# Optimization experiments

Hardware: AMD Instinct MI355X
Metric: run time of the kernel (lower is better)

## Reference

```python
import jax, jax.numpy as jnp
import numpy as np

B, L = 8, 1024
VOCAB = 5000
DW = 256            # d_word_vec = d_model
H = 3 * DW          # hidden_size = 768
NH, HD = 12, 64     # n_head, d_k
D = NH * HD         # 768 = nhead*head_dim
D_INNER = 3072
N_LAYERS = 2
N_HIDDEN = 1024
N_OUT = 5000
MASK = 0
SCALE = 1.0 / float(np.sqrt(HD))


def _sinusoid(n_pos, d_hid):
    pos = np.arange(n_pos, dtype=np.float64)[:, None]
    hid = np.arange(d_hid)[None, :]
    tab = pos / np.power(10000.0, 2 * (hid // 2) / d_hid)
    tab[:, 0::2] = np.sin(tab[:, 0::2])
    tab[:, 1::2] = np.cos(tab[:, 1::2])
    tab[0] = 0.0  # padding_idx=0
    return jnp.asarray(tab, dtype=jnp.float32)


def _ln(x, g, b, eps=1e-5):
    mu = x.mean(-1, keepdims=True)
    var = ((x - mu) ** 2).mean(-1, keepdims=True)
    return (x - mu) * jax.lax.rsqrt(var + eps) * g + b


def _dense(x, w, b):
    # w: [out, in] (torch Conv 1x1 / Linear convention)
    return jnp.einsum('...i,oi->...o', x, w) + b


def _pwff(x, w1, b1, w2, b2, g, bn):
    out = _dense(jax.nn.relu(_dense(x, w1, b1)), w2, b2)
    return _ln(out + x, g, bn)


def _msa1(x, relay, wq, bq, wk, bk, wv, bv, wo, bo):
    # x: [B, L, H] nodes, relay: [B, H]. Star-Transformer ring attention:
    # window = 3 local neighbors + the relay node (4 keys per query).
    Bx, Lx, _ = x.shape
    q = _dense(x, wq, bq).reshape(Bx, Lx, NH, HD)
    k = _dense(x, wk, bk).reshape(Bx, Lx, NH, HD)
    v = _dense(x, wv, bv).reshape(Bx, Lx, NH, HD)
    kp = jnp.pad(k, ((0, 0), (1, 1), (0, 0), (0, 0)))
    vp = jnp.pad(v, ((0, 0), (1, 1), (0, 0), (0, 0)))
    k_win = jnp.stack([kp[:, u:u + Lx] for u in range(3)], axis=2)  # [B,L,3,NH,HD]
    v_win = jnp.stack([vp[:, u:u + Lx] for u in range(3)], axis=2)
    rk = _dense(relay, wk, bk).reshape(Bx, NH, HD)
    rv = _dense(relay, wv, bv).reshape(Bx, NH, HD)
    s_loc = jnp.einsum('blnh,blwnh->blwn', q, k_win)
    s_rel = jnp.einsum('blnh,bnh->bln', q, rk)
    scores = jnp.concatenate([s_loc, s_rel[:, :, None, :]], axis=2) * SCALE  # [B,L,4,NH]
    a = jax.nn.softmax(scores, axis=2)
    att = jnp.einsum('blwn,blwnh->blnh', a[:, :, :3], v_win) + a[:, :, 3][..., None] * rv[:, None]
    return _dense(att.reshape(Bx, Lx, D), wo, bo)


def _msa2(relay, nodes, smask, wq, bq, wk, bk, wv, bv, wo, bo):
    # Satellite->planet global attention: single query (relay) over [relay; nodes].
    Bx = relay.shape[0]
    y = jnp.concatenate([relay[:, None, :], nodes], axis=1)  # [B, 1+L, H]
    q = _dense(relay, wq, bq).reshape(Bx, NH, HD)
    k = _dense(y, wk, bk).reshape(Bx, -1, NH, HD)
    v = _dense(y, wv, bv).reshape(Bx, -1, NH, HD)
    pre = jnp.einsum('bnh,bsnh->bns', q, k) * SCALE
    pre = jnp.where(smask[:, None, :], -jnp.inf, pre)
    a = jax.nn.softmax(pre, axis=2)
    att = jnp.einsum('bns,bsnh->bnh', a, v).reshape(Bx, D)
    return _dense(att, wo, bo)


def setup_inputs():
    ks = iter(jax.random.split(jax.random.key(0), 40))
    def w(shape):
        return jax.random.normal(next(ks), shape, dtype=jnp.float32) * 0.02
    def z(shape):
        return jnp.zeros(shape, jnp.float32)
    def o(shape):
        return jnp.ones(shape, jnp.float32)
    inp = {}
    inp['src_seq'] = jax.random.randint(next(ks), (B, L, 3), 0, VOCAB, dtype=jnp.int32)
    inp['positions'] = jax.random.randint(next(ks), (B,), 0, L, dtype=jnp.int32)
    inp['emb'] = w((VOCAB, DW))
    inp['pos_table'] = _sinusoid(L, H)
    inp['norm_g'] = o((N_LAYERS, H)); inp['norm_b'] = z((N_LAYERS, H))
    inp['pw_w1'] = w((N_LAYERS, D_INNER, H)); inp['pw_b1'] = z((N_LAYERS, D_INNER))
    inp['pw_w2'] = w((N_LAYERS, H, D_INNER)); inp['pw_b2'] = z((N_LAYERS, H))
    inp['pw_g'] = o((N_LAYERS, H)); inp['pw_bn'] = z((N_LAYERS, H))
    for p in ['ring', 'star']:
        inp[p + '_wq'] = w((N_LAYERS, D, H)); inp[p + '_bq'] = z((N_LAYERS, D))
        inp[p + '_wk'] = w((N_LAYERS, D, H)); inp[p + '_bk'] = z((N_LAYERS, D))
        inp[p + '_wv'] = w((N_LAYERS, D, H)); inp[p + '_bv'] = z((N_LAYERS, D))
        inp[p + '_wo'] = w((N_LAYERS, H, D)); inp[p + '_bo'] = z((N_LAYERS, H))
    inp['head_w1'] = w((3, N_HIDDEN, 2 * H)); inp['head_b1'] = z((3, N_HIDDEN))
    inp['head_w2'] = w((3, N_OUT, N_HIDDEN)); inp['head_b2'] = z((3, N_OUT))
    return inp


def reference(src_seq, positions, emb, pos_table, norm_g, norm_b, pw_w1, pw_b1, pw_w2, pw_b2, pw_g, pw_bn, ring_wq, ring_bq, ring_wk, ring_bk, ring_wv, ring_bv, ring_wo, ring_bo, star_wq, star_bq, star_wk, star_bk, star_wv, star_bv, star_wo, star_bo, head_w1, head_b1, head_w2, head_b2):
    Bx, Lx, _ = src_seq.shape
    # [B,L,3,DW] -> [B,L,H], add (frozen) sinusoid positional encoding
    x = emb[src_seq].reshape(Bx, Lx, H) + pos_table[None, :Lx]
    mask_pad = src_seq[:, :, 0] == MASK               # True at padded positions
    smask = jnp.concatenate([jnp.zeros((Bx, 1), bool), mask_pad], axis=1)
    nodes = x
    relay = x.mean(axis=1)                            # [B, H]
    for i in range(N_LAYERS):
        h = _pwff(nodes, pw_w1[i], pw_b1[i], pw_w2[i], pw_b2[i], pw_g[i], pw_bn[i])
        ring = _msa1(h, relay, ring_wq[i], ring_bq[i], ring_wk[i], ring_bk[i], ring_wv[i], ring_bv[i], ring_wo[i], ring_bo[i])
        nodes = jax.nn.leaky_relu(_ln(ring, norm_g[i], norm_b[i]))
        relay = jax.nn.leaky_relu(_msa2(relay, nodes, smask, star_wq[i], star_bq[i], star_wk[i], star_bk[i], star_wv[i], star_bv[i], star_wo[i], star_bo[i]))
        nodes = jnp.where(mask_pad[:, :, None], 0.0, nodes)
    target = nodes[jnp.arange(Bx), positions]         # [B, H]
    ft = jnp.concatenate([relay, target], axis=1)     # [B, 2H]
    outs = [_dense(jax.nn.relu(_dense(ft, head_w1[j], head_b1[j])), head_w2[j], head_b2[j]) for j in range(3)]
    return jnp.concatenate(outs, axis=1).reshape(3 * Bx, N_OUT)
```

## Files before the change

kernel.cpp:

```cpp
#include <hip/hip_runtime.h>
#include <cstdint>
#include <cstddef>


typedef unsigned short u16;
typedef __attribute__((ext_vector_type(4))) float f32x4;
typedef __attribute__((ext_vector_type(8))) __bf16 bf16x8;

#define NB 8
#define SEQ 1024
#define HDIM 768
#define NHEAD 12
#define HD 64
#define DINNER 3072
#define NHID 1024
#define NOUT 5000
#define ATT_SCALE 0.125f

static __device__ __forceinline__ float b2f(u16 u) {
  union { float f; uint32_t i; } v; v.i = ((uint32_t)u) << 16; return v.f;
}
static __device__ __forceinline__ u16 f2b(float f) {
  union { float f; uint32_t i; } v; v.f = f;
  uint32_t r = v.i + 0x7fffu + ((v.i >> 16) & 1u);
  return (u16)(r >> 16);
}
static __device__ __forceinline__ float2 b2f2(uint32_t u) {
  union { float f; uint32_t i; } lo, hi;
  lo.i = u << 16; hi.i = u & 0xffff0000u;
  return make_float2(lo.f, hi.f);
}

static __device__ __forceinline__ void gl2lds16(const void* g, void* l) {
  __builtin_amdgcn_global_load_lds(
      (__attribute__((address_space(1))) void*)(uintptr_t)g,
      (__attribute__((address_space(3))) void*)l, 16, 0, 0);
}

template <int N>
static __device__ __forceinline__ void wait_vmcnt() {
  if constexpr (N == 0) asm volatile("s_waitcnt vmcnt(0)" ::: "memory");
  else if constexpr (N == 3) asm volatile("s_waitcnt vmcnt(3)" ::: "memory");
  else if constexpr (N == 4) asm volatile("s_waitcnt vmcnt(4)" ::: "memory");
  else if constexpr (N == 6) asm volatile("s_waitcnt vmcnt(6)" ::: "memory");
  else if constexpr (N == 8) asm volatile("s_waitcnt vmcnt(8)" ::: "memory");
}

static __device__ __forceinline__ float blk_sum(float v, float* red) {
  #pragma unroll
  for (int off = 32; off > 0; off >>= 1) v += __shfl_down(v, off, 64);
  if ((threadIdx.x & 63) == 0) red[threadIdx.x >> 6] = v;
  __syncthreads();
  float r = red[0] + red[1] + red[2] + red[3];
  __syncthreads();
  return r;
}
static __device__ __forceinline__ float blk_max(float v, float* red) {
  #pragma unroll
  for (int off = 32; off > 0; off >>= 1) v = fmaxf(v, __shfl_down(v, off, 64));
  if ((threadIdx.x & 63) == 0) red[threadIdx.x >> 6] = v;
  __syncthreads();
  float r = fmaxf(fmaxf(red[0], red[1]), fmaxf(red[2], red[3]));
  __syncthreads();
  return r;
}

struct Cvt4 {
  const float* s0; const float* s1; const float* s2; const float* s3;
  u16* d0; u16* d1; u16* d2; u16* d3;
  int c1, c2, c3, c4;
};
__global__ __launch_bounds__(256) void cvt4_k(Cvt4 a) {
  const int i = blockIdx.x * 256 + threadIdx.x;
  if (i >= a.c4) return;
  const float* s; u16* d; int j;
  if (i < a.c1)      { s = a.s0; d = a.d0; j = i; }
  else if (i < a.c2) { s = a.s1; d = a.d1; j = i - a.c1; }
  else if (i < a.c3) { s = a.s2; d = a.d2; j = i - a.c2; }
  else               { s = a.s3; d = a.d3; j = i - a.c3; }
  const float4 v = ((const float4*)s)[j];
  ushort4 o;
  o.x = f2b(v.x); o.y = f2b(v.y); o.z = f2b(v.z); o.w = f2b(v.w);
  ((ushort4*)d)[j] = o;
}

template <int ACT, int TM>
__global__ __launch_bounds__(256) void gemm_bt(
    const u16* __restrict__ A,
    const u16* W0, const u16* W1, const u16* W2,
    const float* b0, const float* b1, const float* b2,
    u16* C0, u16* C1, u16* C2,
    int M, int N, int K) {
  constexpr int MI = TM / 32;
  constexpr int S = TM / 64 + 2;
  __shared__ u16 As[4][TM * 32];
  __shared__ u16 Bs[4][128 * 32];
  const int z = blockIdx.z;
  const u16* W = z == 0 ? W0 : (z == 1 ? W1 : W2);
  const float* bias = z == 0 ? b0 : (z == 1 ? b1 : b2);
  u16* C = z == 0 ? C0 : (z == 1 ? C1 : C2);

  const int tid  = threadIdx.x;
  const int wave = tid >> 6;
  const int lane = tid & 63;
  const int bm = blockIdx.y * TM;
  const int bn = blockIdx.x * 128;
  const int wrq = wave >> 1, wcq = wave & 1;
  const int r16 = lane & 15, quad = lane >> 4;
  const int srow = lane >> 2;
  const int scol = (lane & 3) << 3;

  f32x4 acc[MI][4] = {};

  const int nk = K >> 5;

  auto STAGE = [&](int s, int t) {
    const int k0 = t << 5;
    #pragma unroll
    for (int q = 0; q < TM / 64; ++q) {
      const int rowa = wave * (TM / 4) + q * 16;
      gl2lds16(A + (size_t)(bm + rowa + srow) * K + (k0 + scol),
               (char*)&As[s][0] + (rowa << 6));
    }
    #pragma unroll
    for (int q = 0; q < 2; ++q) {
      const int rowb = wave * 32 + q * 16;
      gl2lds16(W + (size_t)(bn + rowb + srow) * K + (k0 + scol),
               (char*)&Bs[s][0] + (rowb << 6));
    }
  };

  STAGE(0, 0);
  if (1 < nk) STAGE(1, 1);

  for (int t = 0; t < nk; ++t) {
    const int s = t & 3;
    if (t + 2 < nk) {
      STAGE((t + 2) & 3, t + 2);
      __builtin_amdgcn_sched_barrier(0);
      wait_vmcnt<2 * S>();
    } else if (t + 1 < nk) {
      wait_vmcnt<S>();
    } else {
      wait_vmcnt<0>();
    }
    __builtin_amdgcn_sched_barrier(0);
    __builtin_amdgcn_s_barrier();
    __builtin_amdgcn_sched_barrier(0);

    bf16x8 af[MI], bf[4];
    #pragma unroll
    for (int i = 0; i < MI; ++i)
      af[i] = *reinterpret_cast<const bf16x8*>(
          &As[s][(wrq * (TM / 2) + i * 16 + r16) * 32 + quad * 8]);
    #pragma unroll
    for (int j = 0; j < 4; ++j)
      bf[j] = *reinterpret_cast<const bf16x8*>(
          &Bs[s][(wcq * 64 + j * 16 + r16) * 32 + quad * 8]);
    #pragma unroll
    for (int i = 0; i < MI; ++i)
      #pragma unroll
      for (int j = 0; j < 4; ++j)
        acc[i][j] = __builtin_amdgcn_mfma_f32_16x16x32_bf16(af[i], bf[j], acc[i][j], 0, 0, 0);
  }

  #pragma unroll
  for (int j = 0; j < 4; ++j) {
    const int n = bn + wcq * 64 + j * 16 + r16;
    const float bv = bias[n];
    #pragma unroll
    for (int i = 0; i < MI; ++i) {
      const int m0 = bm + wrq * (TM / 2) + i * 16 + quad * 4;
      #pragma unroll
      for (int r = 0; r < 4; ++r) {
        float vv = acc[i][j][r] + bv;
        if (ACT == 1) vv = fmaxf(vv, 0.0f);
        C[(size_t)(m0 + r) * N + n] = f2b(vv);
      }
    }
  }
}

__global__ __launch_bounds__(256) void embed_k(
    const int* __restrict__ src, const float* __restrict__ emb,
    const float* __restrict__ pt, float* __restrict__ x,
    u16* __restrict__ xb) {
  const int r = blockIdx.x;
  const int l = r & (SEQ - 1);
  const int tid = threadIdx.x;
  #pragma unroll
  for (int it = 0; it < 3; ++it) {
    const int idx = tid + it * 256;
    const int c = idx >> 8, d = idx & 255;
    const int tok = src[r * 3 + c];
    const float v = emb[(size_t)tok * 256 + d] + pt[(size_t)l * HDIM + idx];
    x[(size_t)r * HDIM + idx] = v;
    xb[(size_t)r * HDIM + idx] = f2b(v);
  }
}

__global__ __launch_bounds__(256) void relay_mean1_k(
    const float* __restrict__ x, float* __restrict__ part) {
  const int cg = blockIdx.x, seg = blockIdx.y, b = blockIdx.z;
  const int h = cg * 256 + threadIdx.x;
  float s = 0.f;
  const int l0 = seg * 64;
  for (int l = l0; l < l0 + 64; ++l) s += x[((size_t)b * SEQ + l) * HDIM + h];
  part[((size_t)b * 16 + seg) * HDIM + h] = s;
}
__global__ __launch_bounds__(256) void relay_mean2_k(
    const float* __restrict__ part, float* __restrict__ relay) {
  const int b = blockIdx.y;
  const int h = blockIdx.x * 256 + threadIdx.x;
  float s = 0.f;
  #pragma unroll
  for (int i = 0; i < 16; ++i) s += part[((size_t)b * 16 + i) * HDIM + h];
  relay[b * HDIM + h] = s * (1.0f / 1024.0f);
}

__global__ __launch_bounds__(256) void ln_resid_k(
    const u16* __restrict__ pre, const float* __restrict__ res,
    const float* __restrict__ g, const float* __restrict__ bb,
    u16* __restrict__ out) {
  __shared__ float red[4];
  const int r = blockIdx.x;
  const int tid = threadIdx.x;
  const size_t base = (size_t)r * HDIM;
  float v0 = b2f(pre[base + tid])       + res[base + tid];
  float v1 = b2f(pre[base + tid + 256]) + res[base + tid + 256];
  float v2 = b2f(pre[base + tid + 512]) + res[base + tid + 512];
  const float mu = blk_sum(v0 + v1 + v2, red) * (1.0f / 768.0f);
  v0 -= mu; v1 -= mu; v2 -= mu;
  const float var = blk_sum(v0 * v0 + v1 * v1 + v2 * v2, red) * (1.0f / 768.0f);
  const float rs = rsqrtf(var + 1e-5f);
  out[base + tid]       = f2b(v0 * rs * g[tid]       + bb[tid]);
  out[base + tid + 256] = f2b(v1 * rs * g[tid + 256] + bb[tid + 256]);
  out[base + tid + 512] = f2b(v2 * rs * g[tid + 512] + bb[tid + 512]);
}

__global__ __launch_bounds__(256) void ln_leaky_mask_k(
    const u16* __restrict__ pre, const float* __restrict__ g,
    const float* __restrict__ bb, const int* __restrict__ src,
    float* __restrict__ out, u16* __restrict__ outb) {
  __shared__ float red[4];
  const int r = blockIdx.x;
  const int tid = threadIdx.x;
  const size_t base = (size_t)r * HDIM;
  float v0 = b2f(pre[base + tid]);
  float v1 = b2f(pre[base + tid + 256]);
  float v2 = b2f(pre[base + tid + 512]);
  const float mu = blk_sum(v0 + v1 + v2, red) * (1.0f / 768.0f);
  v0 -= mu; v1 -= mu; v2 -= mu;
  const float var = blk_sum(v0 * v0 + v1 * v1 + v2 * v2, red) * (1.0f / 768.0f);
  const float rs = rsqrtf(var + 1e-5f);
  const bool masked = (src[r * 3] == 0);
  float y0 = v0 * rs * g[tid]       + bb[tid];
  float y1 = v1 * rs * g[tid + 256] + bb[tid + 256];
  float y2 = v2 * rs * g[tid + 512] + bb[tid + 512];
  y0 = y0 > 0.f ? y0 : 0.01f * y0;
  y1 = y1 > 0.f ? y1 : 0.01f * y1;
  y2 = y2 > 0.f ? y2 : 0.01f * y2;
  if (masked) { y0 = 0.f; y1 = 0.f; y2 = 0.f; }
  out[base + tid]       = y0;  outb[base + tid]       = f2b(y0);
  out[base + tid + 256] = y1;  outb[base + tid + 256] = f2b(y1);
  out[base + tid + 512] = y2;  outb[base + tid + 512] = f2b(y2);
}

__global__ __launch_bounds__(256) void ring_attn_k(
    const u16* __restrict__ q, const u16* __restrict__ k,
    const u16* __restrict__ v, const float* __restrict__ rk,
    const float* __restrict__ rv, u16* __restrict__ att) {
  __shared__ float qs[HDIM];
  __shared__ float aw[NHEAD][4];
  const int r = blockIdx.x;
  const int b = r >> 10, l = r & (SEQ - 1);
  const int tid = threadIdx.x;
  const size_t base = (size_t)r * HDIM;
  #pragma unroll
  for (int it = 0; it < 3; ++it) {
    const int idx = tid + it * 256;
    qs[idx] = b2f(q[base + idx]);
  }
  __syncthreads();
  if (tid < 192) {
    const int u_ = tid >> 2;
    const int l4 = tid & 3;
    const int n = u_ >> 2, w = u_ & 3;
    const float* qrow = qs + n * HD + l4 * 16;
    float a = 0.f;
    if (w < 3) {
      const int ll = l - 1 + w;
      if (ll >= 0 && ll < SEQ) {
        const uint4* kp4 =
            (const uint4*)(k + base + (size_t)(w - 1) * HDIM + n * HD + l4 * 16);
        #pragma unroll
        for (int t = 0; t < 2; ++t) {
          const uint4 u = kp4[t];
          const float2 f0 = b2f2(u.x), f1 = b2f2(u.y);
          const float2 f2_ = b2f2(u.z), f3 = b2f2(u.w);
          const float* q8 = qrow + t * 8;
          a += q8[0] * f0.x + q8[1] * f0.y + q8[2] * f1.x + q8[3] * f1.y
             + q8[4] * f2_.x + q8[5] * f2_.y + q8[6] * f3.x + q8[7] * f3.y;
        }
      }
    } else {
      const float4* kp4 = (const float4*)(rk + b * HDIM + n * HD + l4 * 16);
      #pragma unroll
      for (int t = 0; t < 4; ++t) {
        const float4 kv = kp4[t];
        const float* q4 = qrow + t * 4;
        a += q4[0] * kv.x + q4[1] * kv.y + q4[2] * kv.z + q4[3] * kv.w;
      }
    }
    a += __shfl_xor(a, 1, 4);
    a += __shfl_xor(a, 2, 4);
    if (l4 == 0) aw[n][w] = a * ATT_SCALE;
  }
  __syncthreads();
  if (tid < NHEAD) {
    const float s0 = aw[tid][0], s1 = aw[tid][1], s2 = aw[tid][2], s3 = aw[tid][3];
    const float m = fmaxf(fmaxf(s0, s1), fmaxf(s2, s3));
    const float e0 = __expf(s0 - m), e1 = __expf(s1 - m);
    const float e2 = __expf(s2 - m), e3 = __expf(s3 - m);
    const float inv = 1.0f / (e0 + e1 + e2 + e3);
    aw[tid][0] = e0 * inv; aw[tid][1] = e1 * inv;
    aw[tid][2] = e2 * inv; aw[tid][3] = e3 * inv;
  }
  __syncthreads();
  #pragma unroll
  for (int it = 0; it < 3; ++it) {
    const int idx = tid + it * 256;
    const int n = idx >> 6;
    float acc = aw[n][3] * rv[b * HDIM + idx];
    if (l > 0)       acc += aw[n][0] * b2f(v[base - HDIM + idx]);
    acc += aw[n][1] * b2f(v[base + idx]);
    if (l < SEQ - 1) acc += aw[n][2] * b2f(v[base + HDIM + idx]);
    att[base + idx] = f2b(acc);
  }
}

__global__ __launch_bounds__(256) void msa2_attn_k(
    const float* __restrict__ q2, const float* __restrict__ rk2,
    const float* __restrict__ rv2, const u16* __restrict__ k2,
    const u16* __restrict__ v2, const int* __restrict__ src,
    float* __restrict__ att) {
  __shared__ float qs[HD];
  __shared__ float sc[SEQ + 1];
  __shared__ float red[4];
  __shared__ float vred[4][HD];
  const int bid = blockIdx.x;
  const int b = bid / NHEAD, n = bid % NHEAD;
  const int tid = threadIdx.x;
  const int hb = b * HDIM + n * HD;
  if (tid < HD) qs[tid] = q2[hb + tid];
  __syncthreads();
  float lmax = -1e30f;
  for (int s = tid; s <= SEQ; s += 256) {
    float sco;
    if (s == 0) {
      float a = 0.f;
      #pragma unroll
      for (int d = 0; d < HD; ++d) a += qs[d] * rk2[hb + d];
      sco = a * ATT_SCALE;
    } else {
      const int l = s - 1;
      if (src[(b * SEQ + l) * 3] == 0) {
        sco = -1e30f;
      } else {
        const uint4* kp4 =
            (const uint4*)(k2 + ((size_t)b * SEQ + l) * HDIM + n * HD);
        float a = 0.f;
        #pragma unroll
        for (int t = 0; t < 8; ++t) {
          const uint4 u = kp4[t];
          const float2 f0 = b2f2(u.x), f1 = b2f2(u.y);
          const float2 f2_ = b2f2(u.z), f3 = b2f2(u.w);
          const float* q8 = qs + t * 8;
          a += q8[0] * f0.x + q8[1] * f0.y + q8[2] * f1.x + q8[3] * f1.y
             + q8[4] * f2_.x + q8[5] * f2_.y + q8[6] * f3.x + q8[7] * f3.y;
        }
        sco = a * ATT_SCALE;
      }
    }
    sc[s] = sco;
    lmax = fmaxf(lmax, sco);
  }
  lmax = blk_max(lmax, red);
  float lsum = 0.f;
  for (int s = tid; s <= SEQ; s += 256) {
    const float e = __expf(sc[s] - lmax);
    sc[s] = e;
    lsum += e;
  }
  lsum = blk_sum(lsum, red);
  {
    const int dd = tid & 63, grp = tid >> 6;
    float acc = 0.f;
    const u16* vp = v2 + (size_t)b * SEQ * HDIM + n * HD + dd;
    for (int l = grp; l < SEQ; l += 4)
      acc += sc[l + 1] * b2f(vp[(size_t)l * HDIM]);
    vred[grp][dd] = acc;
  }
  __syncthreads();
  if (tid < HD) {
    const float inv = 1.0f / lsum;
    const float a = sc[0] * rv2[hb + tid]
                  + vred[0][tid] + vred[1][tid] + vred[2][tid] + vred[3][tid];
    att[hb + tid] = a * inv;
  }
}

__global__ __launch_bounds__(256) void relay_proj_k(
    const float* __restrict__ A, int N, int nm,
    const float* W0, const float* W1, const float* W2,
    const float* b0, const float* b1, const float* b2v,
    float* O0, float* O1, float* O2, int act) {
  const int wid = blockIdx.x * 4 + (threadIdx.x >> 6);
  const int lane = threadIdx.x & 63;
  const int mat = wid / N, n = wid % N;
  const float* W  = mat == 0 ? W0 : (mat == 1 ? W1 : W2);
  const float* bb = mat == 0 ? b0 : (mat == 1 ? b1 : b2v);
  float* O        = mat == 0 ? O0 : (mat == 1 ? O1 : O2);
  const float4* wr = (const float4*)(W + (size_t)n * HDIM);
  float acc[NB] = {};
  #pragma unroll
  for (int it = 0; it < 3; ++it) {
    const int k4 = it * 64 + lane;
    const float4 wv = wr[k4];
    #pragma unroll
    for (int b = 0; b < NB; ++b) {
      const float4 av = *(const float4*)&A[b * HDIM + k4 * 4];
      acc[b] += av.x * wv.x + av.y * wv.y + av.z * wv.z + av.w * wv.w;
    }
  }
  #pragma unroll
  for (int b = 0; b < NB; ++b) {
    float a = acc[b];
    #pragma unroll
    for (int off = 32; off > 0; off >>= 1) a += __shfl_down(a, off, 64);
    if (lane == 0) {
      float v = a + bb[n];
      if (act == 2) v = v > 0.f ? v : 0.01f * v;
      O[(size_t)b * N + n] = v;
    }
  }
}

__global__ __launch_bounds__(256) void ft_k(
    const float* __restrict__ relay, const float* __restrict__ nodes,
    const int* __restrict__ positions, float* __restrict__ ft) {
  const int gid = blockIdx.x * 256 + threadIdx.x;
  const int b = gid / 1536, j = gid % 1536;
  if (j < HDIM) {
    ft[gid] = relay[b * HDIM + j];
  } else {
    const int p = positions[b];
    ft[gid] = nodes[((size_t)b * SEQ + p) * HDIM + (j - HDIM)];
  }
}

__global__ __launch_bounds__(256) void head1_k(
    const float* __restrict__ ft, const float* __restrict__ w,
    const float* __restrict__ bias, float* __restrict__ hid) {
  __shared__ float fs[NB * 1536];
  const int j = blockIdx.y;
  {
    const float4* s4 = (const float4*)ft;
    float4* d4 = (float4*)fs;
    for (int i = threadIdx.x; i < (NB * 1536) / 4; i += 256) d4[i] = s4[i];
  }
  __syncthreads();
  const int wave = threadIdx.x >> 6, lane = threadIdx.x & 63;
  const int o = blockIdx.x * 4 + wave;
  const float4* wr = (const float4*)(w + ((size_t)j * NHID + o) * 1536);
  float acc[NB] = {};
  #pragma unroll
  for (int it = 0; it < 6; ++it) {
    const int k4 = it * 64 + lane;
    const float4 wv = wr[k4];
    #pragma unroll
    for (int b = 0; b < NB; ++b) {
      const float4 hv = *(const float4*)&fs[b * 1536 + k4 * 4];
      acc[b] += hv.x * wv.x + hv.y * wv.y + hv.z * wv.z + hv.w * wv.w;
    }
  }
  #pragma unroll
  for (int b = 0; b < NB; ++b) {
    float a = acc[b];
    #pragma unroll
    for (int off = 32; off > 0; off >>= 1) a += __shfl_down(a, off, 64);
    if (lane == 0)
      hid[((size_t)j * NB + b) * NHID + o] = fmaxf(a + bias[j * NHID + o], 0.f);
  }
}

__global__ __launch_bounds__(256) void head2_k(
    const float* __restrict__ hid, const float* __restrict__ w,
    const float* __restrict__ bias, float* __restrict__ out) {
  __shared__ float hs[NB * NHID];
  const int j = blockIdx.y;
  {
    const float4* s4 = (const float4*)(hid + (size_t)j * NB * NHID);
    float4* d4 = (float4*)hs;
    for (int i = threadIdx.x; i < (NB * NHID) / 4; i += 256) d4[i] = s4[i];
  }
  __syncthreads();
  const int wave = threadIdx.x >> 6, lane = threadIdx.x & 63;
  const int o = blockIdx.x * 4 + wave;
  const float4* wr = (const float4*)(w + ((size_t)j * NOUT + o) * NHID);
  float acc[NB] = {};
  #pragma unroll
  for (int it = 0; it < 4; ++it) {
    const int k4 = it * 64 + lane;
    const float4 wv = wr[k4];
    #pragma unroll
    for (int b = 0; b < NB; ++b) {
      const float4 hv = *(const float4*)&hs[b * NHID + k4 * 4];
      acc[b] += hv.x * wv.x + hv.y * wv.y + hv.z * wv.z + hv.w * wv.w;
    }
  }
  #pragma unroll
  for (int b = 0; b < NB; ++b) {
    float a = acc[b];
    #pragma unroll
    for (int off = 32; off > 0; off >>= 1) a += __shfl_down(a, off, 64);
    if (lane == 0)
      out[(size_t)(b * 3 + j) * NOUT + o] = a + bias[j * NOUT + o];
  }
}

extern "C" void kernel_launch(void* const* d_in, const int* in_sizes, int n_in,
                              void* d_out, int out_size, void* d_ws, size_t ws_size,
                              hipStream_t stream) {
  (void)in_sizes; (void)n_in; (void)out_size; (void)ws_size;
  const int* src       = (const int*)d_in[0];
  const int* positions = (const int*)d_in[1];
  const float* emb   = (const float*)d_in[2];
  const float* pt    = (const float*)d_in[3];
  const float* norm_g = (const float*)d_in[4]; const float* norm_b = (const float*)d_in[5];
  const float* pw_w1 = (const float*)d_in[6];  const float* pw_b1 = (const float*)d_in[7];
  const float* pw_w2 = (const float*)d_in[8];  const float* pw_b2 = (const float*)d_in[9];
  const float* pw_g  = (const float*)d_in[10]; const float* pw_bn = (const float*)d_in[11];
  const float* ring_wq = (const float*)d_in[12]; const float* ring_bq = (const float*)d_in[13];
  const float* ring_wk = (const float*)d_in[14]; const float* ring_bk = (const float*)d_in[15];
  const float* ring_wv = (const float*)d_in[16]; const float* ring_bv = (const float*)d_in[17];
  const float* ring_wo = (const float*)d_in[18]; const float* ring_bo = (const float*)d_in[19];
  const float* star_wq = (const float*)d_in[20]; const float* star_bq = (const float*)d_in[21];
  const float* star_wk = (const float*)d_in[22]; const float* star_bk = (const float*)d_in[23];
  const float* star_wv = (const float*)d_in[24]; const float* star_bv = (const float*)d_in[25];
  const float* star_wo = (const float*)d_in[26]; const float* star_bo = (const float*)d_in[27];
  const float* head_w1 = (const float*)d_in[28]; const float* head_b1 = (const float*)d_in[29];
  const float* head_w2 = (const float*)d_in[30]; const float* head_b2 = (const float*)d_in[31];

  char* ws = (char*)d_ws;
  const size_t NTOK = (size_t)NB * SEQ * HDIM;
  float* nodes   = (float*)(ws);
  u16* preln     = (u16*)(ws + NTOK * 4);
  u16* cbase     = (u16*)(ws + NTOK * 6);
  u16* inner  = cbase;
  u16* slotC0 = cbase;
  u16* slotC1 = cbase + 1 * NTOK;
  u16* slotC2 = cbase + 2 * NTOK;
  u16* slotC3 = cbase + 3 * NTOK;
  u16* shared12  = (u16*)(ws + NTOK * 14);
  u16* wc        = (u16*)(ws + NTOK * 16);
  char* small    = ws + NTOK * 16 + 9437184;
  float* part  = (float*)(small);
  float* relay = (float*)(small + 393216);
  float* sb0 = (float*)(small + 393216 + 1 * 24576);
  float* sb1 = (float*)(small + 393216 + 2 * 24576);
  float* sb2 = (float*)(small + 393216 + 3 * 24576);
  float* sb3 = (float*)(small + 393216 + 4 * 24576);
  float* ftb = (float*)(small + 393216 + 5 * 24576);
  float* hid = (float*)(small + 393216 + 5 * 24576 + 49152);

  u16* nodes_b16 = shared12;
  u16* hbuf      = shared12;

  embed_k<<<NB * SEQ, 256, 0, stream>>>(src, emb, pt, nodes, nodes_b16);
  relay_mean1_k<<<dim3(3, 16, NB), 256, 0, stream>>>(nodes, part);
  relay_mean2_k<<<dim3(3, NB), 256, 0, stream>>>(part, relay);

  const int NW1 = DINNER * HDIM;
  const int NQK = HDIM * HDIM;

  for (int i = 0; i < 2; ++i) {
    const float* pw_w1_l = pw_w1 + (size_t)i * NW1;
    const float* pw_w2_l = pw_w2 + (size_t)i * NW1;
    const float* pw_b1_l = pw_b1 + (size_t)i * DINNER;
    const float* pw_b2_l = pw_b2 + (size_t)i * HDIM;
    const float* pw_g_l  = pw_g + (size_t)i * HDIM;
    const float* pw_bn_l = pw_bn + (size_t)i * HDIM;
    const float* ng_l = norm_g + (size_t)i * HDIM;
    const float* nb_l = norm_b + (size_t)i * HDIM;
    const float* rwq = ring_wq + (size_t)i * NQK; const float* rbq = ring_bq + (size_t)i * HDIM;
    const float* rwk = ring_wk + (size_t)i * NQK; const float* rbk = ring_bk + (size_t)i * HDIM;
    const float* rwv = ring_wv + (size_t)i * NQK; const float* rbv = ring_bv + (size_t)i * HDIM;
    const float* rwo = ring_wo + (size_t)i * NQK; const float* rbo = ring_bo + (size_t)i * HDIM;
    const float* swq = star_wq + (size_t)i * NQK; const float* sbq = star_bq + (size_t)i * HDIM;
    const float* swk = star_wk + (size_t)i * NQK; const float* sbk = star_bk + (size_t)i * HDIM;
    const float* swv = star_wv + (size_t)i * NQK; const float* sbv = star_bv + (size_t)i * HDIM;
    const float* swo = star_wo + (size_t)i * NQK; const float* sbo = star_bo + (size_t)i * HDIM;

    u16* wc_pw1 = wc;
    u16* wc_pw2 = wc + NW1;
    {
      Cvt4 a = { pw_w1_l, pw_w2_l, pw_w1_l, pw_w1_l,
                 wc_pw1, wc_pw2, wc_pw1, wc_pw1,
                 NW1 / 4, NW1 / 2, NW1 / 2, NW1 / 2 };
      cvt4_k<<<(NW1 / 2 + 255) / 256, 256, 0, stream>>>(a);
    }
    gemm_bt<1, 128><<<dim3(DINNER / 128, 64, 1), 256, 0, stream>>>(
        nodes_b16, wc_pw1, wc_pw1, wc_pw1, pw_b1_l, pw_b1_l, pw_b1_l,
        inner, inner, inner, NB * SEQ, DINNER, HDIM);
    gemm_bt<0, 64><<<dim3(HDIM / 128, 128, 1), 256, 0, stream>>>(
        inner, wc_pw2, wc_pw2, wc_pw2, pw_b2_l, pw_b2_l, pw_b2_l,
        preln, preln, preln, NB * SEQ, HDIM, DINNER);
    ln_resid_k<<<NB * SEQ, 256, 0, stream>>>(preln, nodes, pw_g_l, pw_bn_l, hbuf);

    u16* wc_rq = wc;
    u16* wc_rk = wc + NQK;
    u16* wc_rv = wc + 2 * NQK;
    u16* wc_ro = wc + 3 * NQK;
    {
      Cvt4 a = { rwq, rwk, rwv, rwo, wc_rq, wc_rk, wc_rv, wc_ro,
                 NQK / 4, NQK / 2, 3 * NQK / 4, NQK };
      cvt4_k<<<(NQK + 255) / 256, 256, 0, stream>>>(a);
    }
    gemm_bt<0, 64><<<dim3(HDIM / 128, 128, 3), 256, 0, stream>>>(
        hbuf, wc_rq, wc_rk, wc_rv, rbq, rbk, rbv,
        slotC0, slotC1, slotC2, NB * SEQ, HDIM, HDIM);
    relay_proj_k<<<2 * HDIM / 4, 256, 0, stream>>>(
        relay, HDIM, 2, rwk, rwv, rwk, rbk, rbv, rbk, sb0, sb1, sb2, 0);
    ring_attn_k<<<NB * SEQ, 256, 0, stream>>>(slotC0, slotC1, slotC2, sb0, sb1, slotC3);
    gemm_bt<0, 64><<<dim3(HDIM / 128, 128, 1), 256, 0, stream>>>(
        slotC3, wc_ro, wc_ro, wc_ro, rbo, rbo, rbo,
        preln, preln, preln, NB * SEQ, HDIM, HDIM);
    ln_leaky_mask_k<<<NB * SEQ, 256, 0, stream>>>(preln, ng_l, nb_l, src, nodes, nodes_b16);

    u16* wc_sk = wc;
    u16* wc_sv = wc + NQK;
    {
      Cvt4 a = { swk, swv, swk, swk, wc_sk, wc_sv, wc_sk, wc_sk,
                 NQK / 4, NQK / 2, NQK / 2, NQK / 2 };
      cvt4_k<<<(NQK / 2 + 255) / 256, 256, 0, stream>>>(a);
    }
    gemm_bt<0, 64><<<dim3(HDIM / 128, 128, 2), 256, 0, stream>>>(
        nodes_b16, wc_sk, wc_sv, wc_sv, sbk, sbv, sbv,
        slotC0, slotC1, slotC1, NB * SEQ, HDIM, HDIM);
    relay_proj_k<<<3 * HDIM / 4, 256, 0, stream>>>(
        relay, HDIM, 3, swq, swk, swv, sbq, sbk, sbv, sb0, sb1, sb2, 0);
    msa2_attn_k<<<NB * NHEAD, 256, 0, stream>>>(sb0, sb1, sb2, slotC0, slotC1, src, sb3);
    relay_proj_k<<<HDIM / 4, 256, 0, stream>>>(
        sb3, HDIM, 1, swo, swo, swo, sbo, sbo, sbo, relay, sb1, sb2, 2);
  }

  ft_k<<<48, 256, 0, stream>>>(relay, nodes, positions, ftb);
  head1_k<<<dim3(NHID / 4, 3), 256, 0, stream>>>(ftb, head_w1, head_b1, hid);
  head2_k<<<dim3(NOUT / 4, 3), 256, 0, stream>>>(hid, head_w2, head_b2, (float*)d_out);
}
```

Before: 1.087 ms.

## Use 128x128 GEMM tiles with split-K atomics, triple-buffered LDS, repacked layout

Replaces the TM-templated GEMM with a fixed 128x128 tile, three-stage LDS ring buffer, and LDS layout with 16-row subtiles. Issues the next stage's prefetch after the LDS fragment reads. The N=768 GEMMs (pwff second layer and ring output projection) now run split-K=2 with fp32 atomicAdd into a zeroed buffer, and LN kernels read fp32. Multi-matrix QKV batches are folded into blockIdx.x, and workspace buffers are reassigned. This aims to raise data reuse and CU fill for the narrow GEMMs, at the cost of extra zeroing kernels, atomic traffic, and fp32 pre-LN buffers.

```diff
diff --git a/kernel.cpp b/kernel.cpp
--- a/kernel.cpp
+++ b/kernel.cpp
@@ -40,9 +40,7 @@
 template <int N>
 static __device__ __forceinline__ void wait_vmcnt() {
   if constexpr (N == 0) asm volatile("s_waitcnt vmcnt(0)" ::: "memory");
-  else if constexpr (N == 3) asm volatile("s_waitcnt vmcnt(3)" ::: "memory");
   else if constexpr (N == 4) asm volatile("s_waitcnt vmcnt(4)" ::: "memory");
-  else if constexpr (N == 6) asm volatile("s_waitcnt vmcnt(6)" ::: "memory");
   else if constexpr (N == 8) asm volatile("s_waitcnt vmcnt(8)" ::: "memory");
 }
 
@@ -84,81 +82,74 @@
   ((ushort4*)d)[j] = o;
 }
 
-template <int ACT, int TM>
+__global__ __launch_bounds__(256) void zero_k(float4* __restrict__ p) {
+  p[(size_t)blockIdx.x * 256 + threadIdx.x] = make_float4(0.f, 0.f, 0.f, 0.f);
+}
+
+template <int ACT, int SPLITK>
 __global__ __launch_bounds__(256) void gemm_bt(
     const u16* __restrict__ A,
     const u16* W0, const u16* W1, const u16* W2,
     const float* b0, const float* b1, const float* b2,
     u16* C0, u16* C1, u16* C2,
     int M, int N, int K) {
-  constexpr int MI = TM / 32;
-  constexpr int S = TM / 64 + 2;
-  __shared__ u16 As[4][TM * 32];
-  __shared__ u16 Bs[4][128 * 32];
-  const int z = blockIdx.z;
-  const u16* W = z == 0 ? W0 : (z == 1 ? W1 : W2);
-  const float* bias = z == 0 ? b0 : (z == 1 ? b1 : b2);
-  u16* C = z == 0 ? C0 : (z == 1 ? C1 : C2);
+  __shared__ u16 As[3][128 * 32];
+  __shared__ u16 Bs[3][128 * 32];
+  const int nblk = N >> 7;
+  const int mat = (int)blockIdx.x / nblk;
+  const u16* W = mat == 0 ? W0 : (mat == 1 ? W1 : W2);
+  const float* bias = mat == 0 ? b0 : (mat == 1 ? b1 : b2);
+  u16* C = mat == 0 ? C0 : (mat == 1 ? C1 : C2);
 
   const int tid  = threadIdx.x;
   const int wave = tid >> 6;
   const int lane = tid & 63;
-  const int bm = blockIdx.y * TM;
-  const int bn = blockIdx.x * 128;
+  const int bm = blockIdx.y * 128;
+  const int bn = ((int)blockIdx.x - mat * nblk) * 128;
   const int wrq = wave >> 1, wcq = wave & 1;
   const int r16 = lane & 15, quad = lane >> 4;
-  const int srow = lane >> 2;
-  const int scol = (lane & 3) << 3;
-
-  f32x4 acc[MI][4] = {};
-
-  const int nk = K >> 5;
+  const int srow = lane & 15;
+  const int scol = (lane >> 4) << 3;
+
+  const int Ks = K / SPLITK;
+  const int kb = (int)blockIdx.z * Ks;
+  const int nk = Ks >> 5;
+
+  f32x4 acc[4][4] = {};
 
   auto STAGE = [&](int s, int t) {
-    const int k0 = t << 5;
-    #pragma unroll
-    for (int q = 0; q < TM / 64; ++q) {
-      const int rowa = wave * (TM / 4) + q * 16;
-      gl2lds16(A + (size_t)(bm + rowa + srow) * K + (k0 + scol),
-               (char*)&As[s][0] + (rowa << 6));
-    }
+    const int k0 = kb + (t << 5);
     #pragma unroll
     for (int q = 0; q < 2; ++q) {
-      const int rowb = wave * 32 + q * 16;
-      gl2lds16(W + (size_t)(bn + rowb + srow) * K + (k0 + scol),
-               (char*)&Bs[s][0] + (rowb << 6));
+      const int sub = wave * 2 + q;
+      gl2lds16(A + (size_t)(bm + sub * 16 + srow) * K + (k0 + scol),
+               (char*)&As[s][0] + (sub << 10));
+      gl2lds16(W + (size_t)(bn + sub * 16 + srow) * K + (k0 + scol),
+               (char*)&Bs[s][0] + (sub << 10));
     }
   };
 
   STAGE(0, 0);
-  if (1 < nk) STAGE(1, 1);
+  STAGE(1, 1);
 
   for (int t = 0; t < nk; ++t) {
-    const int s = t & 3;
-    if (t + 2 < nk) {
-      STAGE((t + 2) & 3, t + 2);
-      __builtin_amdgcn_sched_barrier(0);
-      wait_vmcnt<2 * S>();
-    } else if (t + 1 < nk) {
-      wait_vmcnt<S>();
-    } else {
-      wait_vmcnt<0>();
-    }
-    __builtin_amdgcn_sched_barrier(0);
+    const int s = t % 3;
+    if (t + 1 < nk) wait_vmcnt<4>(); else wait_vmcnt<0>();
     __builtin_amdgcn_s_barrier();
     __builtin_amdgcn_sched_barrier(0);
-
-    bf16x8 af[MI], bf[4];
-    #pragma unroll
-    for (int i = 0; i < MI; ++i)
+    bf16x8 af[4], bf[4];
+    #pragma unroll
+    for (int i = 0; i < 4; ++i)
       af[i] = *reinterpret_cast<const bf16x8*>(
-          &As[s][(wrq * (TM / 2) + i * 16 + r16) * 32 + quad * 8]);
+          &As[s][((wrq * 4 + i) << 9) + (quad << 7) + (r16 << 3)]);
     #pragma unroll
     for (int j = 0; j < 4; ++j)
       bf[j] = *reinterpret_cast<const bf16x8*>(
-          &Bs[s][(wcq * 64 + j * 16 + r16) * 32 + quad * 8]);
-    #pragma unroll
-    for (int i = 0; i < MI; ++i)
+          &Bs[s][((wcq * 4 + j) << 9) + (quad << 7) + (r16 << 3)]);
+    if (t + 2 < nk) STAGE((t + 2) % 3, t + 2);
+    __builtin_amdgcn_sched_barrier(0);
+    #pragma unroll
+    for (int i = 0; i < 4; ++i)
       #pragma unroll
       for (int j = 0; j < 4; ++j)
         acc[i][j] = __builtin_amdgcn_mfma_f32_16x16x32_bf16(af[i], bf[j], acc[i][j], 0, 0, 0);
@@ -169,13 +160,19 @@
     const int n = bn + wcq * 64 + j * 16 + r16;
     const float bv = bias[n];
     #pragma unroll
-    for (int i = 0; i < MI; ++i) {
-      const int m0 = bm + wrq * (TM / 2) + i * 16 + quad * 4;
+    for (int i = 0; i < 4; ++i) {
+      const int m0 = bm + wrq * 64 + i * 16 + quad * 4;
       #pragma unroll
       for (int r = 0; r < 4; ++r) {
-        float vv = acc[i][j][r] + bv;
-        if (ACT == 1) vv = fmaxf(vv, 0.0f);
-        C[(size_t)(m0 + r) * N + n] = f2b(vv);
+        float vv = acc[i][j][r];
+        if (SPLITK == 1) {
+          vv += bv;
+          if (ACT == 1) vv = fmaxf(vv, 0.0f);
+          C[(size_t)(m0 + r) * N + n] = f2b(vv);
+        } else {
+          if (blockIdx.z == 0) vv += bv;
+          atomicAdd((float*)C + (size_t)(m0 + r) * N + n, vv);
+        }
       }
     }
   }
@@ -219,16 +216,16 @@
 }
 
 __global__ __launch_bounds__(256) void ln_resid_k(
-    const u16* __restrict__ pre, const float* __restrict__ res,
+    const float* __restrict__ pre, const float* __restrict__ res,
     const float* __restrict__ g, const float* __restrict__ bb,
     u16* __restrict__ out) {
   __shared__ float red[4];
   const int r = blockIdx.x;
   const int tid = threadIdx.x;
   const size_t base = (size_t)r * HDIM;
-  float v0 = b2f(pre[base + tid])       + res[base + tid];
-  float v1 = b2f(pre[base + tid + 256]) + res[base + tid + 256];
-  float v2 = b2f(pre[base + tid + 512]) + res[base + tid + 512];
+  float v0 = pre[base + tid]       + res[base + tid];
+  float v1 = pre[base + tid + 256] + res[base + tid + 256];
+  float v2 = pre[base + tid + 512] + res[base + tid + 512];
   const float mu = blk_sum(v0 + v1 + v2, red) * (1.0f / 768.0f);
   v0 -= mu; v1 -= mu; v2 -= mu;
   const float var = blk_sum(v0 * v0 + v1 * v1 + v2 * v2, red) * (1.0f / 768.0f);
@@ -239,16 +236,16 @@
 }
 
 __global__ __launch_bounds__(256) void ln_leaky_mask_k(
-    const u16* __restrict__ pre, const float* __restrict__ g,
+    const float* __restrict__ pre, const float* __restrict__ g,
     const float* __restrict__ bb, const int* __restrict__ src,
     float* __restrict__ out, u16* __restrict__ outb) {
   __shared__ float red[4];
   const int r = blockIdx.x;
   const int tid = threadIdx.x;
   const size_t base = (size_t)r * HDIM;
-  float v0 = b2f(pre[base + tid]);
-  float v1 = b2f(pre[base + tid + 256]);
-  float v2 = b2f(pre[base + tid + 512]);
+  float v0 = pre[base + tid];
+  float v1 = pre[base + tid + 256];
+  float v2 = pre[base + tid + 512];
   const float mu = blk_sum(v0 + v1 + v2, red) * (1.0f / 768.0f);
   v0 -= mu; v1 -= mu; v2 -= mu;
   const float var = blk_sum(v0 * v0 + v1 * v1 + v2 * v2, red) * (1.0f / 768.0f);
@@ -554,17 +551,21 @@
 
   char* ws = (char*)d_ws;
   const size_t NTOK = (size_t)NB * SEQ * HDIM;
+  const size_t U = NTOK * 2;
   float* nodes   = (float*)(ws);
-  u16* preln     = (u16*)(ws + NTOK * 4);
-  u16* cbase     = (u16*)(ws + NTOK * 6);
-  u16* inner  = cbase;
-  u16* slotC0 = cbase;
-  u16* slotC1 = cbase + 1 * NTOK;
-  u16* slotC2 = cbase + 2 * NTOK;
-  u16* slotC3 = cbase + 3 * NTOK;
-  u16* shared12  = (u16*)(ws + NTOK * 14);
-  u16* wc        = (u16*)(ws + NTOK * 16);
-  char* small    = ws + NTOK * 16 + 9437184;
+  u16* inner     = (u16*)(ws + 2 * U);
+  float* prefA   = (float*)(ws + 6 * U);
+  u16* hbuf      = (u16*)(ws + 2 * U);
+  u16* qb        = (u16*)(ws + 3 * U);
+  u16* kb        = (u16*)(ws + 4 * U);
+  u16* vb        = (u16*)(ws + 5 * U);
+  u16* attb      = (u16*)(ws + 6 * U);
+  float* prefB   = (float*)(ws + 2 * U);
+  u16* nodes_b16 = (u16*)(ws + 7 * U);
+  u16* k2b       = (u16*)(ws + 4 * U);
+  u16* v2b       = (u16*)(ws + 5 * U);
+  u16* wc        = (u16*)(ws + 8 * U);
+  char* small    = ws + 8 * U + 9437184;
   float* part  = (float*)(small);
   float* relay = (float*)(small + 393216);
   float* sb0 = (float*)(small + 393216 + 1 * 24576);
@@ -574,15 +575,13 @@
   float* ftb = (float*)(small + 393216 + 5 * 24576);
   float* hid = (float*)(small + 393216 + 5 * 24576 + 49152);
 
-  u16* nodes_b16 = shared12;
-  u16* hbuf      = shared12;
-
   embed_k<<<NB * SEQ, 256, 0, stream>>>(src, emb, pt, nodes, nodes_b16);
   relay_mean1_k<<<dim3(3, 16, NB), 256, 0, stream>>>(nodes, part);
   relay_mean2_k<<<dim3(3, NB), 256, 0, stream>>>(part, relay);
 
   const int NW1 = DINNER * HDIM;
   const int NQK = HDIM * HDIM;
+  const int M = NB * SEQ;
 
   for (int i = 0; i < 2; ++i) {
     const float* pw_w1_l = pw_w1 + (size_t)i * NW1;
@@ -610,13 +609,14 @@
                  NW1 / 4, NW1 / 2, NW1 / 2, NW1 / 2 };
       cvt4_k<<<(NW1 / 2 + 255) / 256, 256, 0, stream>>>(a);
     }
-    gemm_bt<1, 128><<<dim3(DINNER / 128, 64, 1), 256, 0, stream>>>(
+    gemm_bt<1, 1><<<dim3(DINNER / 128, M / 128, 1), 256, 0, stream>>>(
         nodes_b16, wc_pw1, wc_pw1, wc_pw1, pw_b1_l, pw_b1_l, pw_b1_l,
-        inner, inner, inner, NB * SEQ, DINNER, HDIM);
-    gemm_bt<0, 64><<<dim3(HDIM / 128, 128, 1), 256, 0, stream>>>(
+        inner, inner, inner, M, DINNER, HDIM);
+    zero_k<<<(int)(NTOK / 1024), 256, 0, stream>>>((float4*)prefA);
+    gemm_bt<0, 2><<<dim3(HDIM / 128, M / 128, 2), 256, 0, stream>>>(
         inner, wc_pw2, wc_pw2, wc_pw2, pw_b2_l, pw_b2_l, pw_b2_l,
-        preln, preln, preln, NB * SEQ, HDIM, DINNER);
-    ln_resid_k<<<NB * SEQ, 256, 0, stream>>>(preln, nodes, pw_g_l, pw_bn_l, hbuf);
+        (u16*)prefA, (u16*)prefA, (u16*)prefA, M, HDIM, DINNER);
+    ln_resid_k<<<M, 256, 0, stream>>>(prefA, nodes, pw_g_l, pw_bn_l, hbuf);
 
     u16* wc_rq = wc;
     u16* wc_rk = wc + NQK;
@@ -627,16 +627,17 @@
                  NQK / 4, NQK / 2, 3 * NQK / 4, NQK };
       cvt4_k<<<(NQK + 255) / 256, 256, 0, stream>>>(a);
     }
-    gemm_bt<0, 64><<<dim3(HDIM / 128, 128, 3), 256, 0, stream>>>(
+    gemm_bt<0, 1><<<dim3(3 * (HDIM / 128), M / 128, 1), 256, 0, stream>>>(
         hbuf, wc_rq, wc_rk, wc_rv, rbq, rbk, rbv,
-        slotC0, slotC1, slotC2, NB * SEQ, HDIM, HDIM);
+        qb, kb, vb, M, HDIM, HDIM);
     relay_proj_k<<<2 * HDIM / 4, 256, 0, stream>>>(
         relay, HDIM, 2, rwk, rwv, rwk, rbk, rbv, rbk, sb0, sb1, sb2, 0);
-    ring_attn_k<<<NB * SEQ, 256, 0, stream>>>(slotC0, slotC1, slotC2, sb0, sb1, slotC3);
-    gemm_bt<0, 64><<<dim3(HDIM / 128, 128, 1), 256, 0, stream>>>(
-        slotC3, wc_ro, wc_ro, wc_ro, rbo, rbo, rbo,
-        preln, preln, preln, NB * SEQ, HDIM, HDIM);
-    ln_leaky_mask_k<<<NB * SEQ, 256, 0, stream>>>(preln, ng_l, nb_l, src, nodes, nodes_b16);
+    ring_attn_k<<<NB * SEQ, 256, 0, stream>>>(qb, kb, vb, sb0, sb1, attb);
+    zero_k<<<(int)(NTOK / 1024), 256, 0, stream>>>((float4*)prefB);
+    gemm_bt<0, 2><<<dim3(HDIM / 128, M / 128, 2), 256, 0, stream>>>(
+        attb, wc_ro, wc_ro, wc_ro, rbo, rbo, rbo,
+        (u16*)prefB, (u16*)prefB, (u16*)prefB, M, HDIM, HDIM);
+    ln_leaky_mask_k<<<M, 256, 0, stream>>>(prefB, ng_l, nb_l, src, nodes, nodes_b16);
 
     u16* wc_sk = wc;
     u16* wc_sv = wc + NQK;
@@ -645,12 +646,12 @@
                  NQK / 4, NQK / 2, NQK / 2, NQK / 2 };
       cvt4_k<<<(NQK / 2 + 255) / 256, 256, 0, stream>>>(a);
     }
-    gemm_bt<0, 64><<<dim3(HDIM / 128, 128, 2), 256, 0, stream>>>(
+    gemm_bt<0, 1><<<dim3(2 * (HDIM / 128), M / 128, 1), 256, 0, stream>>>(
         nodes_b16, wc_sk, wc_sv, wc_sv, sbk, sbv, sbv,
-        slotC0, slotC1, slotC1, NB * SEQ, HDIM, HDIM);
+        k2b, v2b, v2b, M, HDIM, HDIM);
     relay_proj_k<<<3 * HDIM / 4, 256, 0, stream>>>(
         relay, HDIM, 3, swq, swk, swv, sbq, sbk, sbv, sb0, sb1, sb2, 0);
-    msa2_attn_k<<<NB * NHEAD, 256, 0, stream>>>(sb0, sb1, sb2, slotC0, slotC1, src, sb3);
+    msa2_attn_k<<<NB * NHEAD, 256, 0, stream>>>(sb0, sb1, sb2, k2b, v2b, src, sb3);
     relay_proj_k<<<HDIM / 4, 256, 0, stream>>>(
         sb3, HDIM, 1, swo, swo, swo, sbo, sbo, sbo, relay, sb1, sb2, 2);
   }
```

Result: slower. 1.273 ms (+17.1%).
